# Optimization experiments

Measured on AMD Instinct MI355X. Metric: run time of the kernel, lower is better.

The kernel has to match this reference:

```python
import jax, jax.numpy as jnp
import numpy as np

B, D, K, A, P = 4096, 512, 128, 32, 16  # batch, theta dim, mixture comps, alpha dim, hutchinson probes


def setup_inputs() -> dict:
    key = jax.random.key(0)
    k1, k2, k3, k4 = jax.random.split(key, 4)
    thetas = jax.random.normal(k1, (B, D), dtype=jnp.float32)
    alpha = jax.random.normal(k2, (K, A), dtype=jnp.float32)
    W = jax.random.normal(k3, (A, D), dtype=jnp.float32) / jnp.sqrt(jnp.float32(A))
    v_int = jax.random.randint(k4, (P, B, D), 0, 2, dtype=jnp.int32)  # -> Rademacher via 2v-1
    return {"thetas": thetas, "alpha": alpha, "W": W, "v_int": v_int,
            "N_dataset": 100000, "K_alpha_samples": K}


def _log_density(thetas, alpha, W, N_dataset, K_alpha):
    # Tempered Gaussian mixture: mu_k = alpha_k @ W;
    # logp_b = (N/(N+1)) * (logsumexp_k -0.5||theta_b - mu_k||^2 - log K)
    mu = alpha @ W                                        # [K, D]
    # ||t - mu||^2 expanded to avoid a [B,K,D] intermediate
    sq = (jnp.sum(thetas * thetas, -1, keepdims=True)
          - 2.0 * thetas @ mu.T
          + jnp.sum(mu * mu, -1)[None, :])                # [B, K]
    temper = jnp.float32(N_dataset) / (jnp.float32(N_dataset) + 1.0)
    return temper * (jax.nn.logsumexp(-0.5 * sq, axis=1) - jnp.log(jnp.float32(K_alpha)))


def reference(thetas, alpha, W, v_int, N_dataset, K_alpha_samples):
    v = (2 * v_int - 1).astype(thetas.dtype)              # [P, B, D] Rademacher

    def logp_sum(t):
        return jnp.sum(_log_density(t, alpha, W, N_dataset, K_alpha_samples))

    score = jax.grad(logp_sum)                            # gradiente wrt thetas
    g = score(thetas)                                     # [B, D]

    # Hutchinson trace of the per-sample Hessian via forward-over-reverse HVPs,
    # batched over probes (fuses the torch per-probe autograd.grad loop).
    def hvp(vi):
        return jax.jvp(score, (thetas,), (vi,))[1]        # [B, D]

    Hv = jax.vmap(hvp)(v)                                 # [P, B, D]
    traces = jnp.mean(jnp.sum(v * Hv, axis=-1), axis=0)   # [B]

    loss = 0.5 * jnp.sum(g * g, axis=-1) + traces         # [B]
    return jnp.mean(loss)
```

## Files before the change

### kernel.cpp

```cpp
#include <hip/hip_runtime.h>
#include <hip/hip_bf16.h>
#include <stdint.h>

#define Bsz 4096
#define Dn  512
#define Kn  128
#define Pn  16
#define An  32
#define TB  16

typedef __attribute__((ext_vector_type(4))) float  floatx4;
typedef __attribute__((ext_vector_type(8))) short  shortx8;

__device__ unsigned short g_mu_bf[Kn * Dn];
__device__ unsigned short g_mu_t[Dn * Kn];
__device__ float          g_munorm[Kn];

__device__ __forceinline__ unsigned short f2bf(float x) {
    union { float f; uint32_t u; } v; v.f = x;
    uint32_t u = v.u;
    uint32_t r = (u + 0x7FFFu + ((u >> 16) & 1u)) >> 16;
    return (unsigned short)r;
}

__device__ __forceinline__ float rowsum16(float x) {
    x += __int_as_float(__builtin_amdgcn_update_dpp(0, __float_as_int(x), 0xB1, 0xF, 0xF, false));
    x += __int_as_float(__builtin_amdgcn_update_dpp(0, __float_as_int(x), 0x4E, 0xF, 0xF, false));
    x += __int_as_float(__builtin_amdgcn_update_dpp(0, __float_as_int(x), 0x124, 0xF, 0xF, false));
    x += __int_as_float(__builtin_amdgcn_update_dpp(0, __float_as_int(x), 0x128, 0xF, 0xF, false));
    return x;
}

__global__ __launch_bounds__(256) void k_mu(const float* __restrict__ alpha,
                                            const float* __restrict__ W,
                                            float* __restrict__ out) {
    __shared__ float al[An];
    __shared__ float red[4];
    int k = blockIdx.x, t = threadIdx.x;
    if (k == 0 && t == 0) *out = 0.f;
    if (t < An) al[t] = alpha[k * An + t];
    __syncthreads();
    int d0 = t, d1 = t + 256;
    float a0 = 0.f, a1 = 0.f;
#pragma unroll
    for (int a = 0; a < An; ++a) {
        float av = al[a];
        a0 = fmaf(av, W[a * Dn + d0], a0);
        a1 = fmaf(av, W[a * Dn + d1], a1);
    }
    unsigned short h0 = f2bf(a0), h1 = f2bf(a1);
    g_mu_bf[k * Dn + d0] = h0;  g_mu_bf[k * Dn + d1] = h1;
    g_mu_t[d0 * Kn + k] = h0;   g_mu_t[d1 * Kn + k] = h1;
    float nrm = a0 * a0 + a1 * a1;
#pragma unroll
    for (int msk = 1; msk < 64; msk <<= 1) nrm += __shfl_xor(nrm, msk);
    if ((t & 63) == 0) red[t >> 6] = nrm;
    __syncthreads();
    if (t == 0) g_munorm[k] = red[0] + red[1] + red[2] + red[3];
}

__global__ __launch_bounds__(512, 4) void k_main(
    const float* __restrict__ thetas,
    const int* __restrict__ v_int,
    const int* __restrict__ Np,
    float* __restrict__ out)
{
    __shared__ short vt[2][TB][520];
    __shared__ float S_l[TB][132];
    __shared__ float w_l[TB][132];
    __shared__ short wbf[TB][136];
    __shared__ float part[2][8][TB][2];
    __shared__ float thn[TB];
    __shared__ float SwS[TB];

    const int tid = threadIdx.x;
    const int lane = tid & 63;
    const int wv = tid >> 6;
    const int m = lane & 15;
    const int q = lane >> 4;

    const int tileb = blockIdx.x >> 1;
    const int phalf = blockIdx.x & 1;
    const int b0 = tileb * TB;
    const int p0 = phalf * 8;

    const float Nf = (float)(*Np);
    const float temper = Nf / (Nf + 1.0f);

    const int kcol = wv * 16 + m;
    shortx8 mufrag[16];
    {
        const unsigned short* mb = g_mu_bf + (size_t)kcol * Dn + q * 8;
#pragma unroll
        for (int dc = 0; dc < 16; ++dc)
            mufrag[dc] = *(const shortx8*)(mb + dc * 32);
    }

    const int r = tid >> 5;
    const int c0 = (tid & 31) * 16;
    const size_t PB = (size_t)Bsz * Dn;
    const int* vrow = v_int + (size_t)(b0 + r) * Dn + c0;

    int4 buf[4];
    {
        const int4* g = (const int4*)(vrow + (size_t)p0 * PB);
#pragma unroll
        for (int j = 0; j < 4; ++j) buf[j] = g[j];
    }
    {
        const float4* tg = (const float4*)(thetas + (size_t)(b0 + r) * Dn + c0);
        float tn = 0.f;
#pragma unroll
        for (int j = 0; j < 4; ++j) {
            float4 f = tg[j];
            tn += f.x * f.x + f.y * f.y + f.z * f.z + f.w * f.w;
            short4 h;
            h.x = (short)f2bf(f.x); h.y = (short)f2bf(f.y);
            h.z = (short)f2bf(f.z); h.w = (short)f2bf(f.w);
            *(short4*)&vt[0][r][c0 + j * 4] = h;
        }
#pragma unroll
        for (int msk = 1; msk < 32; msk <<= 1) tn += __shfl_xor(tn, msk);
        if ((tid & 31) == 0) thn[r] = tn;
    }
    __syncthreads();

    {
        floatx4 acc = {0.f, 0.f, 0.f, 0.f};
#pragma unroll
        for (int dc = 0; dc < 16; ++dc) {
            shortx8 a = *(const shortx8*)&vt[0][m][dc * 32 + q * 8];
            acc = __builtin_amdgcn_mfma_f32_16x16x32_bf16(a, mufrag[dc], acc, 0, 0, 0);
        }
#pragma unroll
        for (int i = 0; i < 4; ++i) S_l[q * 4 + i][kcol] = acc[i];
    }
    __syncthreads();

    {
        const int b = tid >> 5, s = tid & 31;
        float l[4];
        float mx = -3.4e38f;
        float tnb = thn[b];
#pragma unroll
        for (int j = 0; j < 4; ++j) {
            int k = s + 32 * j;
            l[j] = -0.5f * (tnb - 2.f * S_l[b][k] + g_munorm[k]);
            mx = fmaxf(mx, l[j]);
        }
#pragma unroll
        for (int msk = 1; msk < 32; msk <<= 1) mx = fmaxf(mx, __shfl_xor(mx, msk));
        float se = 0.f, ses = 0.f;
        float e[4];
#pragma unroll
        for (int j = 0; j < 4; ++j) {
            int k = s + 32 * j;
            e[j] = __expf(l[j] - mx);
            se += e[j];
            ses += e[j] * S_l[b][k];
        }
#pragma unroll
        for (int msk = 1; msk < 32; msk <<= 1) { se += __shfl_xor(se, msk); ses += __shfl_xor(ses, msk); }
        float inv = 1.f / se;
#pragma unroll
        for (int j = 0; j < 4; ++j) {
            int k = s + 32 * j;
            float wvv = e[j] * inv;
            w_l[b][k] = wvv;
            wbf[b][k] = (short)f2bf(wvv);
        }
        if (s == 0) SwS[b] = ses * inv;
    }
    __syncthreads();

    {
        float sg[4] = {0.f, 0.f, 0.f, 0.f};
#pragma unroll
        for (int ct = 0; ct < 4; ++ct) {
            const unsigned short* mt = g_mu_t + (size_t)(wv * 64 + ct * 16 + m) * Kn + q * 8;
            floatx4 acc = {0.f, 0.f, 0.f, 0.f};
#pragma unroll
            for (int kc = 0; kc < 4; ++kc) {
                shortx8 a = *(const shortx8*)&wbf[m][kc * 32 + q * 8];
                shortx8 bfr = *(const shortx8*)(mt + kc * 32);
                acc = __builtin_amdgcn_mfma_f32_16x16x32_bf16(a, bfr, acc, 0, 0, 0);
            }
#pragma unroll
            for (int i = 0; i < 4; ++i) sg[i] += acc[i] * acc[i];
        }
#pragma unroll
        for (int i = 0; i < 4; ++i) sg[i] = rowsum16(sg[i]);
        if (m == 0) {
#pragma unroll
            for (int i = 0; i < 4; ++i) part[0][wv][q * 4 + i][0] = sg[i];
        }
    }

    float wt4[4];
#pragma unroll
    for (int i = 0; i < 4; ++i) wt4[i] = w_l[q * 4 + i][kcol];
    __syncthreads();

    float lossA = 0.f, tracc = 0.f;
    if (tid < TB) {
        float wGw = 0.f;
#pragma unroll
        for (int w8 = 0; w8 < 8; ++w8) wGw += part[0][w8][tid][0];
        if (phalf == 0)
            lossA = 0.5f * temper * temper * (wGw - 2.f * SwS[tid] + thn[tid])
                    - temper * (float)Dn;
    }

#pragma unroll
    for (int p = 0; p < 8; ++p) {
#pragma unroll
        for (int j = 0; j < 2; ++j) {
            int4 a = buf[2 * j], b = buf[2 * j + 1];
            uint32_t l0 = 0xBF80BF80u ^ ((uint32_t)a.x << 15) ^ ((uint32_t)a.y << 31);
            uint32_t l1 = 0xBF80BF80u ^ ((uint32_t)a.z << 15) ^ ((uint32_t)a.w << 31);
            uint32_t l2 = 0xBF80BF80u ^ ((uint32_t)b.x << 15) ^ ((uint32_t)b.y << 31);
            uint32_t l3 = 0xBF80BF80u ^ ((uint32_t)b.z << 15) ^ ((uint32_t)b.w << 31);
            uint4 pk; pk.x = l0; pk.y = l1; pk.z = l2; pk.w = l3;
            *(uint4*)&vt[p & 1][r][c0 + j * 8] = pk;
        }
        __syncthreads();
        if (p < 7) {
            const int4* g = (const int4*)(vrow + (size_t)(p0 + p + 1) * PB);
#pragma unroll
            for (int j = 0; j < 4; ++j) buf[j] = g[j];
        }
        if (p > 0 && tid < TB) {
            float S1 = 0.f, S2 = 0.f;
#pragma unroll
            for (int w8 = 0; w8 < 8; ++w8) {
                S1 += part[(p - 1) & 1][w8][tid][0];
                S2 += part[(p - 1) & 1][w8][tid][1];
            }
            tracc += S1 - S2 * S2;
        }
        floatx4 acc = {0.f, 0.f, 0.f, 0.f};
#pragma unroll
        for (int dc = 0; dc < 16; ++dc) {
            shortx8 a = *(const shortx8*)&vt[p & 1][m][dc * 32 + q * 8];
            acc = __builtin_amdgcn_mfma_f32_16x16x32_bf16(a, mufrag[dc], acc, 0, 0, 0);
        }
        float s1[4], s2[4];
#pragma unroll
        for (int i = 0; i < 4; ++i) {
            float T = acc[i];
            s1[i] = wt4[i] * T * T;
            s2[i] = wt4[i] * T;
        }
#pragma unroll
        for (int i = 0; i < 4; ++i) {
            s1[i] = rowsum16(s1[i]);
            s2[i] = rowsum16(s2[i]);
        }
        if (m == 0) {
#pragma unroll
            for (int i = 0; i < 4; ++i) {
                part[p & 1][wv][q * 4 + i][0] = s1[i];
                part[p & 1][wv][q * 4 + i][1] = s2[i];
            }
        }
    }
    __syncthreads();
    if (tid < TB) {
        float S1 = 0.f, S2 = 0.f;
#pragma unroll
        for (int w8 = 0; w8 < 8; ++w8) {
            S1 += part[1][w8][tid][0];
            S2 += part[1][w8][tid][1];
        }
        tracc += S1 - S2 * S2;
        float res = temper * tracc * (1.0f / (float)Pn) + lossA;
#pragma unroll
        for (int msk = 1; msk < 16; msk <<= 1) res += __shfl_xor(res, msk);
        if (tid == 0) atomicAdd(out, res * (1.0f / (float)Bsz));
    }
}

extern "C" void kernel_launch(void* const* d_in, const int* in_sizes, int n_in,
                              void* d_out, int out_size, void* d_ws, size_t ws_size,
                              hipStream_t stream) {
    const float* thetas = (const float*)d_in[0];
    const float* alpha  = (const float*)d_in[1];
    const float* W      = (const float*)d_in[2];
    const int*   v_int  = (const int*)d_in[3];
    const int*   Np     = (const int*)d_in[4];
    (void)d_ws; (void)ws_size;

    float* out = (float*)d_out;
    k_mu  <<<dim3(Kn),  dim3(256), 0, stream>>>(alpha, W, out);
    k_main<<<dim3(512), dim3(512), 0, stream>>>(thetas, v_int, Np, out);
}
```

Baseline: 219.5 us.

## Split fused kernel into softmax-weight kernel and per-probe streaming MFMA kernel

Splits the main kernel in two. The first computes the mixture weights and the score term and writes the weights to a global buffer. The second gives each wave 16 batch rows of a single probe and streams the Rademacher int data straight from global memory into MFMA A-fragments, with register prefetch and no shared-memory staging or per-probe block barriers. In exchange it adds a kernel launch, a global round-trip for the weights, and repeated reads of mu from global/L2 inside the inner loop.

Measured after the change: 255.1 us. 1.16x slower.

```diff
diff --git a/kernel.cpp b/kernel.cpp
--- a/kernel.cpp
+++ b/kernel.cpp
@@ -15,6 +15,7 @@
 __device__ unsigned short g_mu_bf[Kn * Dn];
 __device__ unsigned short g_mu_t[Dn * Kn];
 __device__ float          g_munorm[Kn];
+__device__ float          g_w[Bsz * Kn];
 
 __device__ __forceinline__ unsigned short f2bf(float x) {
     union { float f; uint32_t u; } v; v.f = x;
@@ -59,17 +60,14 @@
     if (t == 0) g_munorm[k] = red[0] + red[1] + red[2] + red[3];
 }
 
-__global__ __launch_bounds__(512, 4) void k_main(
-    const float* __restrict__ thetas,
-    const int* __restrict__ v_int,
-    const int* __restrict__ Np,
-    float* __restrict__ out)
-{
-    __shared__ short vt[2][TB][520];
+__global__ __launch_bounds__(512) void k_w(const float* __restrict__ thetas,
+                                           const int* __restrict__ Np,
+                                           float* __restrict__ out) {
+    __shared__ short vt[TB][520];
     __shared__ float S_l[TB][132];
     __shared__ float w_l[TB][132];
     __shared__ short wbf[TB][136];
-    __shared__ float part[2][8][TB][2];
+    __shared__ float part8[8][TB];
     __shared__ float thn[TB];
     __shared__ float SwS[TB];
 
@@ -78,11 +76,7 @@
     const int wv = tid >> 6;
     const int m = lane & 15;
     const int q = lane >> 4;
-
-    const int tileb = blockIdx.x >> 1;
-    const int phalf = blockIdx.x & 1;
-    const int b0 = tileb * TB;
-    const int p0 = phalf * 8;
+    const int b0 = blockIdx.x * TB;
 
     const float Nf = (float)(*Np);
     const float temper = Nf / (Nf + 1.0f);
@@ -98,15 +92,6 @@
 
     const int r = tid >> 5;
     const int c0 = (tid & 31) * 16;
-    const size_t PB = (size_t)Bsz * Dn;
-    const int* vrow = v_int + (size_t)(b0 + r) * Dn + c0;
-
-    int4 buf[4];
-    {
-        const int4* g = (const int4*)(vrow + (size_t)p0 * PB);
-#pragma unroll
-        for (int j = 0; j < 4; ++j) buf[j] = g[j];
-    }
     {
         const float4* tg = (const float4*)(thetas + (size_t)(b0 + r) * Dn + c0);
         float tn = 0.f;
@@ -117,7 +102,7 @@
             short4 h;
             h.x = (short)f2bf(f.x); h.y = (short)f2bf(f.y);
             h.z = (short)f2bf(f.z); h.w = (short)f2bf(f.w);
-            *(short4*)&vt[0][r][c0 + j * 4] = h;
+            *(short4*)&vt[r][c0 + j * 4] = h;
         }
 #pragma unroll
         for (int msk = 1; msk < 32; msk <<= 1) tn += __shfl_xor(tn, msk);
@@ -129,7 +114,7 @@
         floatx4 acc = {0.f, 0.f, 0.f, 0.f};
 #pragma unroll
         for (int dc = 0; dc < 16; ++dc) {
-            shortx8 a = *(const shortx8*)&vt[0][m][dc * 32 + q * 8];
+            shortx8 a = *(const shortx8*)&vt[m][dc * 32 + q * 8];
             acc = __builtin_amdgcn_mfma_f32_16x16x32_bf16(a, mufrag[dc], acc, 0, 0, 0);
         }
 #pragma unroll
@@ -168,6 +153,7 @@
             float wvv = e[j] * inv;
             w_l[b][k] = wvv;
             wbf[b][k] = (short)f2bf(wvv);
+            g_w[(size_t)(b0 + b) * Kn + k] = wvv;
         }
         if (s == 0) SwS[b] = ses * inv;
     }
@@ -192,91 +178,102 @@
         for (int i = 0; i < 4; ++i) sg[i] = rowsum16(sg[i]);
         if (m == 0) {
 #pragma unroll
-            for (int i = 0; i < 4; ++i) part[0][wv][q * 4 + i][0] = sg[i];
-        }
-    }
-
-    float wt4[4];
-#pragma unroll
-    for (int i = 0; i < 4; ++i) wt4[i] = w_l[q * 4 + i][kcol];
-    __syncthreads();
-
-    float lossA = 0.f, tracc = 0.f;
+            for (int i = 0; i < 4; ++i) part8[wv][q * 4 + i] = sg[i];
+        }
+    }
+    __syncthreads();
+
     if (tid < TB) {
         float wGw = 0.f;
 #pragma unroll
-        for (int w8 = 0; w8 < 8; ++w8) wGw += part[0][w8][tid][0];
-        if (phalf == 0)
-            lossA = 0.5f * temper * temper * (wGw - 2.f * SwS[tid] + thn[tid])
+        for (int w8 = 0; w8 < 8; ++w8) wGw += part8[w8][tid];
+        float res = 0.5f * temper * temper * (wGw - 2.f * SwS[tid] + thn[tid])
                     - temper * (float)Dn;
-    }
-
-#pragma unroll
-    for (int p = 0; p < 8; ++p) {
-#pragma unroll
-        for (int j = 0; j < 2; ++j) {
-            int4 a = buf[2 * j], b = buf[2 * j + 1];
-            uint32_t l0 = 0xBF80BF80u ^ ((uint32_t)a.x << 15) ^ ((uint32_t)a.y << 31);
-            uint32_t l1 = 0xBF80BF80u ^ ((uint32_t)a.z << 15) ^ ((uint32_t)a.w << 31);
-            uint32_t l2 = 0xBF80BF80u ^ ((uint32_t)b.x << 15) ^ ((uint32_t)b.y << 31);
-            uint32_t l3 = 0xBF80BF80u ^ ((uint32_t)b.z << 15) ^ ((uint32_t)b.w << 31);
-            uint4 pk; pk.x = l0; pk.y = l1; pk.z = l2; pk.w = l3;
-            *(uint4*)&vt[p & 1][r][c0 + j * 8] = pk;
-        }
-        __syncthreads();
-        if (p < 7) {
-            const int4* g = (const int4*)(vrow + (size_t)(p0 + p + 1) * PB);
-#pragma unroll
-            for (int j = 0; j < 4; ++j) buf[j] = g[j];
-        }
-        if (p > 0 && tid < TB) {
-            float S1 = 0.f, S2 = 0.f;
-#pragma unroll
-            for (int w8 = 0; w8 < 8; ++w8) {
-                S1 += part[(p - 1) & 1][w8][tid][0];
-                S2 += part[(p - 1) & 1][w8][tid][1];
-            }
-            tracc += S1 - S2 * S2;
-        }
-        floatx4 acc = {0.f, 0.f, 0.f, 0.f};
-#pragma unroll
-        for (int dc = 0; dc < 16; ++dc) {
-            shortx8 a = *(const shortx8*)&vt[p & 1][m][dc * 32 + q * 8];
-            acc = __builtin_amdgcn_mfma_f32_16x16x32_bf16(a, mufrag[dc], acc, 0, 0, 0);
-        }
-        float s1[4], s2[4];
-#pragma unroll
-        for (int i = 0; i < 4; ++i) {
-            float T = acc[i];
-            s1[i] = wt4[i] * T * T;
-            s2[i] = wt4[i] * T;
-        }
-#pragma unroll
-        for (int i = 0; i < 4; ++i) {
-            s1[i] = rowsum16(s1[i]);
-            s2[i] = rowsum16(s2[i]);
-        }
-        if (m == 0) {
-#pragma unroll
-            for (int i = 0; i < 4; ++i) {
-                part[p & 1][wv][q * 4 + i][0] = s1[i];
-                part[p & 1][wv][q * 4 + i][1] = s2[i];
-            }
-        }
-    }
-    __syncthreads();
-    if (tid < TB) {
-        float S1 = 0.f, S2 = 0.f;
-#pragma unroll
-        for (int w8 = 0; w8 < 8; ++w8) {
-            S1 += part[1][w8][tid][0];
-            S2 += part[1][w8][tid][1];
-        }
-        tracc += S1 - S2 * S2;
-        float res = temper * tracc * (1.0f / (float)Pn) + lossA;
 #pragma unroll
         for (int msk = 1; msk < 16; msk <<= 1) res += __shfl_xor(res, msk);
         if (tid == 0) atomicAdd(out, res * (1.0f / (float)Bsz));
+    }
+}
+
+__global__ __launch_bounds__(512, 4) void k_probe(const int* __restrict__ v_int,
+                                                  const int* __restrict__ Np,
+                                                  float* __restrict__ out) {
+    __shared__ float partial[8];
+
+    const int tid = threadIdx.x;
+    const int lane = tid & 63;
+    const int w = tid >> 6;
+    const int m = lane & 15;
+    const int q = lane >> 4;
+
+    const int bid = blockIdx.x;
+    const int probe = bid >> 5;
+    const int btile = bid & 31;
+    const int r0 = btile * 128 + w * 16;
+
+    const float Nf = (float)(*Np);
+    const float temper = Nf / (Nf + 1.0f);
+
+    const size_t PB = (size_t)Bsz * Dn;
+    const char* vg = (const char*)(v_int + (size_t)probe * PB + (size_t)(r0 + m) * Dn) + q * 32;
+    const unsigned short* mub = g_mu_bf + (size_t)m * Dn + q * 8;
+
+    int4 vb[4][2];
+#pragma unroll
+    for (int c = 0; c < 4; ++c) {
+        vb[c][0] = *(const int4*)(vg + c * 128);
+        vb[c][1] = *(const int4*)(vg + c * 128 + 16);
+    }
+
+    floatx4 acc[8];
+#pragma unroll
+    for (int kt = 0; kt < 8; ++kt) acc[kt] = (floatx4){0.f, 0.f, 0.f, 0.f};
+
+#pragma unroll
+    for (int dc = 0; dc < 16; ++dc) {
+        int4 w0 = vb[dc & 3][0], w1 = vb[dc & 3][1];
+        if (dc < 12) {
+            vb[dc & 3][0] = *(const int4*)(vg + (dc + 4) * 128);
+            vb[dc & 3][1] = *(const int4*)(vg + (dc + 4) * 128 + 16);
+        }
+        union { uint32_t u[4]; shortx8 s; } af;
+        af.u[0] = 0xBF80BF80u ^ ((uint32_t)w0.x << 15) ^ ((uint32_t)w0.y << 31);
+        af.u[1] = 0xBF80BF80u ^ ((uint32_t)w0.z << 15) ^ ((uint32_t)w0.w << 31);
+        af.u[2] = 0xBF80BF80u ^ ((uint32_t)w1.x << 15) ^ ((uint32_t)w1.y << 31);
+        af.u[3] = 0xBF80BF80u ^ ((uint32_t)w1.z << 15) ^ ((uint32_t)w1.w << 31);
+#pragma unroll
+        for (int kt = 0; kt < 8; ++kt) {
+            shortx8 bf = *(const shortx8*)(mub + (size_t)kt * 16 * Dn + dc * 32);
+            acc[kt] = __builtin_amdgcn_mfma_f32_16x16x32_bf16(af.s, bf, acc[kt], 0, 0, 0);
+        }
+    }
+
+    float contrib = 0.f;
+#pragma unroll
+    for (int i = 0; i < 4; ++i) {
+        const float* wrow = g_w + (size_t)(r0 + q * 4 + i) * Kn + m;
+        float s1 = 0.f, s2 = 0.f;
+#pragma unroll
+        for (int kt = 0; kt < 8; ++kt) {
+            float T = acc[kt][i];
+            float ww = wrow[kt * 16];
+            s1 = fmaf(ww * T, T, s1);
+            s2 = fmaf(ww, T, s2);
+        }
+        s1 = rowsum16(s1);
+        s2 = rowsum16(s2);
+        contrib += s1 - s2 * s2;
+    }
+    if (m != 0) contrib = 0.f;
+    contrib += __shfl_xor(contrib, 16);
+    contrib += __shfl_xor(contrib, 32);
+    if (lane == 0) partial[w] = contrib;
+    __syncthreads();
+    if (tid == 0) {
+        float t = 0.f;
+#pragma unroll
+        for (int i = 0; i < 8; ++i) t += partial[i];
+        atomicAdd(out, t * temper * (1.0f / (float)Pn) * (1.0f / (float)Bsz));
     }
 }
 
@@ -291,6 +288,7 @@
     (void)d_ws; (void)ws_size;
 
     float* out = (float*)d_out;
-    k_mu  <<<dim3(Kn),  dim3(256), 0, stream>>>(alpha, W, out);
-    k_main<<<dim3(512), dim3(512), 0, stream>>>(thetas, v_int, Np, out);
-}
+    k_mu   <<<dim3(Kn),  dim3(256), 0, stream>>>(alpha, W, out);
+    k_w    <<<dim3(256), dim3(512), 0, stream>>>(thetas, Np, out);
+    k_probe<<<dim3(512), dim3(512), 0, stream>>>(v_int, Np, out);
+}
```
